# Optimization experiments

Measured on AMD Instinct MI355X. Metric: run time of the kernel, lower is better.

Reference implementation:

```python
import jax, jax.numpy as jnp
import numpy as np

N = 20000   # nodes
E = 400000  # edges per hop
IN_C = 256
HID = 128
HEADS = 2
OUT_C = 256
RELU_SLOPE = 0.2  # GATConv LeakyReLU negative slope
EPS = 1e-16


def _segment_mean(vals, idx, num_segments):
    s = jax.ops.segment_sum(vals, idx, num_segments=num_segments)
    cnt = jax.ops.segment_sum(jnp.ones((vals.shape[0], 1), vals.dtype), idx,
                              num_segments=num_segments)
    return s / (cnt + EPS)


def _gat(x, src, dst, Wg, a_src, a_dst, bg):
    # x: [N, IN_C] -> h: [N, HEADS, HID]
    h = (x @ Wg).reshape(N, HEADS, HID)
    alpha_s = jnp.sum(h * a_src, axis=-1)  # [N, HEADS]
    alpha_d = jnp.sum(h * a_dst, axis=-1)  # [N, HEADS]
    logits = jax.nn.leaky_relu(alpha_s[src] + alpha_d[dst], RELU_SLOPE)  # [E, HEADS]
    # softmax over incoming edges per destination node
    m = jax.ops.segment_max(logits, dst, num_segments=N)  # [N, HEADS]
    m = jnp.where(jnp.isfinite(m), m, 0.0)
    ex = jnp.exp(logits - m[dst])
    denom = jax.ops.segment_sum(ex, dst, num_segments=N)  # [N, HEADS]
    alpha = ex / (denom[dst] + EPS)  # [E, HEADS]
    msg = h[src] * alpha[..., None]  # [E, HEADS, HID]
    out = jax.ops.segment_sum(msg, dst, num_segments=N)  # [N, HEADS, HID]
    return out.reshape(N, HEADS * HID) + bg


def setup_inputs() -> dict:
    key = jax.random.key(0)
    ks = jax.random.split(key, 16)

    def xav(k, shape):
        fan_in, fan_out = shape[0], shape[-1]
        lim = np.sqrt(6.0 / (fan_in + fan_out)).astype(np.float32)
        return jax.random.uniform(k, shape, jnp.float32, -lim, lim)

    inp = {
        "x": jax.random.normal(ks[0], (N, IN_C), jnp.float32),
        "edge_index_1hop": jax.random.randint(ks[1], (2, E), 0, N),
        "edge_time_1hop": jax.random.uniform(ks[2], (E,), jnp.float32),
        "edge_index_2hop": jax.random.randint(ks[3], (2, E), 0, N),
        "edge_time_2hop": jax.random.uniform(ks[4], (E,), jnp.float32),
        "rel_embeddings": jax.random.normal(ks[5], (N, HID), jnp.float32),
        # GATConv params
        "Wg": xav(ks[6], (IN_C, HEADS * HID)),
        "a_src": jax.random.normal(ks[7], (HEADS, HID), jnp.float32) * 0.1,
        "a_dst": jax.random.normal(ks[8], (HEADS, HID), jnp.float32) * 0.1,
        "bg": jnp.zeros((HEADS * HID,), jnp.float32),
        # linear_transform
        "W_lin": xav(ks[9], (HEADS * HID, OUT_C)),
        "b_lin": jnp.zeros((OUT_C,), jnp.float32),
        # time_gate: in = 2*(OUT_C+1)
        "W_tg": xav(ks[10], (2 * (OUT_C + 1), 1)),
        "b_tg": jnp.zeros((1,), jnp.float32),
        # semantic_gate: in = (OUT_C+1) + HID + 1
        "W_sg": xav(ks[11], (OUT_C + 1 + HID + 1, 1)),
        "b_sg": jnp.zeros((1,), jnp.float32),
    }
    return inp


def reference(x, edge_index_1hop, edge_time_1hop, edge_index_2hop,
              edge_time_2hop, rel_embeddings, Wg, a_src, a_dst, bg,
              W_lin, b_lin, W_tg, b_tg, W_sg, b_sg):
    src1, dst1 = edge_index_1hop[0], edge_index_1hop[1]
    src2, dst2 = edge_index_2hop[0], edge_index_2hop[1]

    # ---- 1-hop aggregation ----
    x_1hop = _gat(x, src1, dst1, Wg, a_src, a_dst, bg) @ W_lin + b_lin  # [N, OUT_C]
    time_e1 = edge_time_1hop[:, None]  # [E, 1]
    node_time = _segment_mean(time_e1, dst1, N)  # [N, 1]
    x_1hop_t = jnp.concatenate([x_1hop, node_time], axis=-1)  # [N, OUT_C+1]

    # ---- semantic gate (per 1-hop edge -> per node) ----
    combined = jnp.concatenate(
        [x_1hop_t[src1], rel_embeddings[dst1], time_e1], axis=-1)  # [E, OUT_C+1+HID+1]
    sem_w_edge = jax.nn.sigmoid(combined @ W_sg + b_sg)  # [E, 1]
    sem_w_node = _segment_mean(sem_w_edge, dst1, N)  # [N, 1]

    # ---- 2-hop aggregation, semantically weighted ----
    x_2hop = _gat(x, src2, dst2, Wg, a_src, a_dst, bg) @ W_lin + b_lin  # [N, OUT_C]
    x_2hop = x_2hop * sem_w_node
    x_2hop_t = jnp.concatenate([x_2hop, node_time], axis=-1)  # [N, OUT_C+1]

    # ---- time-gated fusion ----
    gate_in = jnp.concatenate([x_1hop_t, x_2hop_t], axis=-1)  # [N, 2*(OUT_C+1)]
    g = jax.nn.sigmoid(gate_in @ W_tg + b_tg)  # [N, 1]
    return g * x_2hop_t + (1.0 - g) * x_1hop_t
```

## Files before the change

### kernel.cpp

```cpp
#include <hip/hip_runtime.h>
#include <math.h>

constexpr float EPSF = 1e-16f;
#define MAXDEG 64
#define BINCH 4096
#define NBUCK 64

typedef __attribute__((ext_vector_type(8))) short bfrag;
typedef __attribute__((ext_vector_type(4))) float ffrag;
typedef __attribute__((ext_vector_type(2))) float f32x2;
typedef __attribute__((ext_vector_type(8))) unsigned short ushortv8;

__device__ __forceinline__ float leaky(float v){ return v >= 0.f ? v : 0.2f*v; }

__device__ __forceinline__ ushort f2bf(float f){
  union { float f; unsigned u; } v; v.f = f;
  unsigned r = (v.u + 0x7FFFu + ((v.u >> 16) & 1u)) >> 16;
  return (ushort)r;
}
__device__ __forceinline__ float bf2f(ushort u){
  union { unsigned u; float f; } v; v.u = ((unsigned)u) << 16;
  return v.f;
}
__device__ __forceinline__ float asf(unsigned u){
  union { unsigned u; float f; } v; v.u = u; return v.f;
}

__device__ __forceinline__ float wred_max(float v){
  #pragma unroll
  for (int d = 32; d; d >>= 1) v = fmaxf(v, __shfl_xor(v, d));
  return v;
}
__device__ __forceinline__ float wred_sum(float v){
  #pragma unroll
  for (int d = 32; d; d >>= 1) v += __shfl_xor(v, d);
  return v;
}


__global__ __launch_bounds__(256) void k_prep(const float* __restrict__ Wg, const float* __restrict__ Wlin,
    const float* __restrict__ blin, const float* __restrict__ rel, const float* __restrict__ Wsg,
    ushort* __restrict__ Wgt, ushort* __restrict__ Wlt, float* __restrict__ p2,
    float* __restrict__ wv, float* __restrict__ wvc,
    float4* __restrict__ zbase, int znum4, int ZB, int N){
  __shared__ float tile[32][33];
  int b = blockIdx.x, t = threadIdx.x;
  if (b < ZB){
    int idx = b*256 + t;
    if (idx < znum4) zbase[idx] = make_float4(0.f,0.f,0.f,0.f);
  } else if (b < ZB + 128){
    int bb = b - ZB;
    const float* W = (bb < 64) ? Wg : Wlin;
    ushort* Wt = (bb < 64) ? Wgt : Wlt;
    bb &= 63;
    int bx = (bb & 7)*32, by = (bb >> 3)*32;
    int tx = t & 31, ty = t >> 5;
    for (int r = ty; r < 32; r += 8) tile[r][tx] = W[(size_t)(by+r)*256 + bx+tx];
    __syncthreads();
    for (int r = ty; r < 32; r += 8) Wt[(size_t)(bx+r)*256 + by+tx] = f2bf(tile[tx][r]);
  } else if (b == ZB + 128){
    __shared__ float sWsg[256];
    __shared__ float wsum[4];
    sWsg[t] = Wsg[t];
    __syncthreads();
    float acc = 0.f;
    const float* row = Wlin + (size_t)t*256;
    for (int c = 0; c < 256; c += 4){
      acc = fmaf(row[c],   sWsg[c],   acc);
      acc = fmaf(row[c+1], sWsg[c+1], acc);
      acc = fmaf(row[c+2], sWsg[c+2], acc);
      acc = fmaf(row[c+3], sWsg[c+3], acc);
    }
    wv[t] = acc;
    float pc = blin[t]*sWsg[t];
    pc = wred_sum(pc);
    if ((t & 63) == 0) wsum[t >> 6] = pc;
    __syncthreads();
    if (t == 0) wvc[0] = wsum[0] + wsum[1] + wsum[2] + wsum[3];
  } else {
    int node = (b-ZB-129)*4 + (t>>6);
    if (node >= N) return;
    int lane = t & 63;
    const float* rr = rel + (size_t)node*128;
    float q = rr[lane]*Wsg[257+lane] + rr[64+lane]*Wsg[321+lane];
    q = wred_sum(q);
    if (lane == 0) p2[node] = q;
  }
}


__global__ __launch_bounds__(256) void k_work1(const float* __restrict__ x, const ushort* __restrict__ Wgt,
    const float* __restrict__ a_src, const float* __restrict__ a_dst,
    ushort* __restrict__ hb, float* __restrict__ as_, float* __restrict__ ad_,
    const int* __restrict__ ei1, const float* __restrict__ et1, const int* __restrict__ ei2,
    int* __restrict__ gcur, int2* __restrict__ bkt1, int2* __restrict__ bkt2,
    int cap1, int cap2, int N, int E1, int E2, int GB1, int B1, int NB){
  __shared__ int hist[NBUCK];
  __shared__ int loff[NBUCK+1];
  __shared__ int cur[NBUCK];
  __shared__ int gbase_s[NBUCK];
  __shared__ int2 stage[BINCH];
  int bid = blockIdx.x, t = threadIdx.x;
  if (bid >= GB1){
    int hop = (bid >= GB1 + B1);
    int cb  = hop ? (bid - GB1 - B1) : (bid - GB1);
    const int* src_arr = hop ? ei2 : ei1;
    const int* dst_arr = hop ? (ei2 + E2) : (ei1 + E1);
    int Eh = hop ? E2 : E1;
    int c0 = cb * BINCH;
    int M = Eh - c0; if (M > BINCH) M = BINCH;
    if (t < NBUCK) hist[t] = 0;
    __syncthreads();
    #pragma unroll
    for (int k = 0; k < BINCH/256; k++){
      int i = k*256 + t;
      if (i < M) atomicAdd(&hist[dst_arr[c0 + i] / NB], 1);
    }
    __syncthreads();
    if (t < NBUCK){
      int v = hist[t];
      int xx = v;
      #pragma unroll
      for (int d = 1; d < NBUCK; d <<= 1){
        int y = __shfl_up(xx, d);
        if (t >= d) xx += y;
      }
      loff[t+1] = xx;
      if (t == 0) loff[0] = 0;
      cur[t] = xx - v;
      gbase_s[t] = atomicAdd(&gcur[hop*NBUCK + t], v);
    }
    __syncthreads();
    #pragma unroll
    for (int k = 0; k < BINCH/256; k++){
      int i = k*256 + t;
      if (i < M){
        int s = src_arr[c0 + i];
        int d = dst_arr[c0 + i];
        int b = d / NB;
        int ld = d - b*NB;
        int pos = atomicAdd(&cur[b], 1);
        float tv = hop ? 0.f : et1[c0 + i];
        stage[pos] = make_int2(s | (ld << 15), __float_as_int(tv));
      }
    }
    __syncthreads();
    int2* bkt = hop ? bkt2 : bkt1;
    int cap = hop ? cap2 : cap1;
    for (int s = t; s < M; s += 256){
      int lo = 0, hi = NBUCK;
      while (hi - lo > 1){ int mid = (lo + hi) >> 1; if (loff[mid] <= s) lo = mid; else hi = mid; }
      int gpos = gbase_s[lo] + (s - loff[lo]);
      if (gpos < cap) bkt[(size_t)lo*cap + gpos] = stage[s];
    }
    return;
  }
  int head = bid & 1;
  int bx = bid >> 1;
  int wid = t >> 6, lane = t & 63;
  int wr = wid >> 1, wc = wid & 1;
  int row0 = bx*128 + wr*64;
  int col0 = head*128 + wc*64;
  int l15 = lane & 15, lk = lane >> 4;
  ffrag acc[4][4];
  #pragma unroll
  for (int i = 0; i < 4; i++)
    #pragma unroll
    for (int j = 0; j < 4; j++){ ffrag z; z[0]=0.f; z[1]=0.f; z[2]=0.f; z[3]=0.f; acc[i][j] = z; }
  for (int kk = 0; kk < 256; kk += 32){
    bfrag a[4], b[4];
    #pragma unroll
    for (int i = 0; i < 4; i++){
      int r = row0 + i*16 + l15; if (r > N-1) r = N-1;
      float4 u0 = *(const float4*)(x + (size_t)r*256 + kk + lk*8);
      float4 u1 = *(const float4*)(x + (size_t)r*256 + kk + lk*8 + 4);
      bfrag tv;
      tv[0]=(short)f2bf(u0.x); tv[1]=(short)f2bf(u0.y); tv[2]=(short)f2bf(u0.z); tv[3]=(short)f2bf(u0.w);
      tv[4]=(short)f2bf(u1.x); tv[5]=(short)f2bf(u1.y); tv[6]=(short)f2bf(u1.z); tv[7]=(short)f2bf(u1.w);
      a[i] = tv;
      int c = col0 + i*16 + l15;
      b[i] = *(const bfrag*)(Wgt + (size_t)c*256 + kk + lk*8);
    }
    #pragma unroll
    for (int i = 0; i < 4; i++)
      #pragma unroll
      for (int j = 0; j < 4; j++)
        acc[i][j] = __builtin_amdgcn_mfma_f32_16x16x32_bf16(a[i], b[j], acc[i][j], 0, 0, 0);
  }
  float asv[4], adv[4];
  #pragma unroll
  for (int j = 0; j < 4; j++){
    int cc = wc*64 + j*16 + l15;
    asv[j] = a_src[head*128 + cc];
    adv[j] = a_dst[head*128 + cc];
  }
  #pragma unroll
  for (int i = 0; i < 4; i++){
    float ps[4] = {0.f,0.f,0.f,0.f}, pd[4] = {0.f,0.f,0.f,0.f};
    #pragma unroll
    for (int j = 0; j < 4; j++){
      int c = col0 + j*16 + l15;
      #pragma unroll
      for (int q = 0; q < 4; q++){
        int r = row0 + i*16 + lk*4 + q;
        float v = acc[i][j][q];
        if (r < N) hb[(size_t)r*256 + c] = f2bf(v);
        ps[q] = fmaf(v, asv[j], ps[q]);
        pd[q] = fmaf(v, adv[j], pd[q]);
      }
    }
    #pragma unroll
    for (int q = 0; q < 4; q++){
      #pragma unroll
      for (int d = 1; d < 16; d <<= 1){
        ps[q] += __shfl_xor(ps[q], d);
        pd[q] += __shfl_xor(pd[q], d);
      }
      int r = row0 + i*16 + lk*4 + q;
      if (l15 == 0 && r < N){
        atomicAdd(&as_[r*2 + head], ps[q]);
        atomicAdd(&ad_[r*2 + head], pd[q]);
      }
    }
  }
}


__global__ __launch_bounds__(256) void k_place(const int* __restrict__ gcur,
    const int2* __restrict__ bkt1, const int2* __restrict__ bkt2, int cap1, int cap2,
    int* __restrict__ ssrc1, int* __restrict__ ssrc2, float* __restrict__ stime1,
    int* __restrict__ cntg, float* __restrict__ ntime, int N, int NB){
  __shared__ int   cnt_l[512];
  __shared__ float ts_l[512];
  int b = blockIdx.x & 63, hop = blockIdx.x >> 6;
  int t = threadIdx.x;
  int nbase = b * NB;
  int ncnt = N - nbase; if (ncnt > NB) ncnt = NB; if (ncnt < 0) ncnt = 0;
  for (int i = t; i < NB; i += 256){ cnt_l[i] = 0; ts_l[i] = 0.f; }
  __syncthreads();
  const int2* bkt = hop ? bkt2 : bkt1;
  int cap = hop ? cap2 : cap1;
  int len = gcur[hop*NBUCK + b]; if (len > cap) len = cap;
  int* ssrc = hop ? ssrc2 : ssrc1;
  for (int i = t; i < len; i += 256){
    int2 en = bkt[(size_t)b*cap + i];
    int src = en.x & 0x7FFF;
    int ld  = en.x >> 15;
    int slot = atomicAdd(&cnt_l[ld], 1);
    if (slot < MAXDEG){
      size_t o = (size_t)(nbase + ld)*MAXDEG + slot;
      ssrc[o] = src;
      if (hop == 0) stime1[o] = __int_as_float(en.y);
    }
    if (hop == 0) atomicAdd(&ts_l[ld], __int_as_float(en.y));
  }
  __syncthreads();
  for (int ld = t; ld < ncnt; ld += 256){
    int node = nbase + ld;
    int c = cnt_l[ld];
    cntg[hop*N + node] = c;
    if (hop == 0) ntime[node] = ts_l[ld] / ((float)c + EPSF);
  }
}


__global__ __launch_bounds__(256) void k_node(const int* __restrict__ cntg,
    const int* __restrict__ ssrc1, const int* __restrict__ ssrc2,
    const float* __restrict__ as_, const float* __restrict__ ad_,
    const ushort* __restrict__ h, const float* __restrict__ bg,
    const float* __restrict__ wv, const float* __restrict__ wvc,
    const float* __restrict__ Wsg, const float* __restrict__ ntime,
    ushort* __restrict__ gatb, float* __restrict__ p1, int N, int gN4){
  __shared__ int   s_src[4][MAXDEG];
  __shared__ float s_wf[4][2][MAXDEG];
  int wid = threadIdx.x >> 6, lane = threadIdx.x & 63;
  int hop = blockIdx.x >= gN4;
  int node = (blockIdx.x - (hop ? gN4 : 0))*4 + wid;
  bool active = node < N;
  const int* ssrc = hop ? ssrc2 : ssrc1;
  int deg = 0; float ad0 = 0.f, ad1 = 0.f;
  if (active){
    int degt = cntg[hop*N + node];
    deg = degt > MAXDEG ? MAXDEG : degt;
    ad0 = ad_[node*2]; ad1 = ad_[node*2+1];
  }
  size_t o0 = (size_t)node * MAXDEG;
  int msrc = 0;
  float l0 = -INFINITY, l1 = -INFINITY;
  if (lane < deg){
    msrc = ssrc[o0 + lane];
    float2 a = ((const float2*)as_)[msrc];
    l0 = leaky(a.x + ad0); l1 = leaky(a.y + ad1);
  }
  float m0 = wred_max(l0), m1 = wred_max(l1);
  float x0 = 0.f, x1 = 0.f;
  if (lane < deg){ x0 = __expf(l0 - m0); x1 = __expf(l1 - m1); }
  float e0 = wred_sum(x0), e1 = wred_sum(x1);
  s_src[wid][lane] = msrc;
  s_wf[wid][0][lane] = x0 / (e0 + EPSF);
  s_wf[wid][1][lane] = x1 / (e1 + EPSF);
  if (!active) return;
  int eh = lane >> 5, cl = lane & 31, ch0 = cl << 3, head = cl >> 4;
  const float* wrow = s_wf[wid][head];
  const int*   srow = s_src[wid];
  f32x2 acc2[4];
  #pragma unroll
  for (int j = 0; j < 4; j++){ acc2[j][0] = 0.f; acc2[j][1] = 0.f; }
  union UV { ushortv8 v; unsigned d[4]; };
  int i = 0;
  for (; i + 8 <= deg; i += 8){
    int eA = i + eh, eB = i + 2 + eh, eC = i + 4 + eh, eD = i + 6 + eh;
    int sA = srow[eA], sB = srow[eB], sC = srow[eC], sD = srow[eD];
    float wA = wrow[eA], wB = wrow[eB], wC = wrow[eC], wD = wrow[eD];
    UV uA, uB, uC, uD;
    uA.v = *(const ushortv8*)(h + (size_t)sA*256 + ch0);
    uB.v = *(const ushortv8*)(h + (size_t)sB*256 + ch0);
    uC.v = *(const ushortv8*)(h + (size_t)sC*256 + ch0);
    uD.v = *(const ushortv8*)(h + (size_t)sD*256 + ch0);
    f32x2 wA2 = {wA,wA}, wB2 = {wB,wB}, wC2 = {wC,wC}, wD2 = {wD,wD};
    #pragma unroll
    for (int j = 0; j < 4; j++){
      f32x2 hv;
      hv[0] = asf(uA.d[j] << 16); hv[1] = asf(uA.d[j] & 0xffff0000u);
      acc2[j] += hv * wA2;
    }
    #pragma unroll
    for (int j = 0; j < 4; j++){
      f32x2 hv;
      hv[0] = asf(uB.d[j] << 16); hv[1] = asf(uB.d[j] & 0xffff0000u);
      acc2[j] += hv * wB2;
    }
    #pragma unroll
    for (int j = 0; j < 4; j++){
      f32x2 hv;
      hv[0] = asf(uC.d[j] << 16); hv[1] = asf(uC.d[j] & 0xffff0000u);
      acc2[j] += hv * wC2;
    }
    #pragma unroll
    for (int j = 0; j < 4; j++){
      f32x2 hv;
      hv[0] = asf(uD.d[j] << 16); hv[1] = asf(uD.d[j] & 0xffff0000u);
      acc2[j] += hv * wD2;
    }
  }
  for (; i < deg; i += 2){
    int e = i + eh;
    bool v = e < deg;
    int s = v ? srow[e] : 0;
    float w = v ? wrow[e] : 0.f;
    UV u; u.v = *(const ushortv8*)(h + (size_t)s*256 + ch0);
    f32x2 w2 = {w, w};
    #pragma unroll
    for (int j = 0; j < 4; j++){
      f32x2 hv;
      hv[0] = asf(u.d[j] << 16); hv[1] = asf(u.d[j] & 0xffff0000u);
      acc2[j] += hv * w2;
    }
  }
  #pragma unroll
  for (int j = 0; j < 4; j++){
    acc2[j][0] += __shfl_xor(acc2[j][0], 32);
    acc2[j][1] += __shfl_xor(acc2[j][1], 32);
  }
  if (eh == 0){
    float4 b0 = *(const float4*)(bg + ch0);
    float4 b1 = *(const float4*)(bg + ch0 + 4);
    float a8[8];
    a8[0] = acc2[0][0] + b0.x; a8[1] = acc2[0][1] + b0.y;
    a8[2] = acc2[1][0] + b0.z; a8[3] = acc2[1][1] + b0.w;
    a8[4] = acc2[2][0] + b1.x; a8[5] = acc2[2][1] + b1.y;
    a8[6] = acc2[3][0] + b1.z; a8[7] = acc2[3][1] + b1.w;
    ushortv8 o;
    #pragma unroll
    for (int k = 0; k < 8; k++) o[k] = f2bf(a8[k]);
    *(ushortv8*)(gatb + (size_t)(hop ? N + node : node)*256 + ch0) = o;
    if (hop == 0){
      float vs = 0.f;
      const float* wvp = wv + ch0;
      #pragma unroll
      for (int k = 0; k < 8; k++) vs = fmaf(a8[k], wvp[k], vs);
      #pragma unroll
      for (int d = 16; d; d >>= 1) vs += __shfl_xor(vs, d);
      if (cl == 0) p1[node] = vs + wvc[0] + ntime[node]*Wsg[256];
    }
  }
}


__global__ __launch_bounds__(256) void k_gemm2(const ushort* __restrict__ A, const ushort* __restrict__ Bt,
    const float* __restrict__ bias, ushort* __restrict__ Cb, int M){
  int wid = threadIdx.x >> 6, lane = threadIdx.x & 63;
  int wr = wid >> 1, wc = wid & 1;
  int row0 = blockIdx.x*128 + wr*64;
  int col0 = blockIdx.y*128 + wc*64;
  int l15 = lane & 15, lk = lane >> 4;
  ffrag acc[4][4];
  #pragma unroll
  for (int i = 0; i < 4; i++)
    #pragma unroll
    for (int j = 0; j < 4; j++){ ffrag z; z[0]=0.f; z[1]=0.f; z[2]=0.f; z[3]=0.f; acc[i][j] = z; }
  for (int kk = 0; kk < 256; kk += 32){
    bfrag a[4], b[4];
    #pragma unroll
    for (int i = 0; i < 4; i++){
      int r = row0 + i*16 + l15; if (r > M-1) r = M-1;
      a[i] = *(const bfrag*)(A + (size_t)r*256 + kk + lk*8);
      int c = col0 + i*16 + l15;
      b[i] = *(const bfrag*)(Bt + (size_t)c*256 + kk + lk*8);
    }
    #pragma unroll
    for (int i = 0; i < 4; i++)
      #pragma unroll
      for (int j = 0; j < 4; j++)
        acc[i][j] = __builtin_amdgcn_mfma_f32_16x16x32_bf16(a[i], b[j], acc[i][j], 0, 0, 0);
  }
  float bv[4];
  #pragma unroll
  for (int j = 0; j < 4; j++) bv[j] = bias[col0 + j*16 + l15];
  #pragma unroll
  for (int i = 0; i < 4; i++){
    #pragma unroll
    for (int j = 0; j < 4; j++){
      int c = col0 + j*16 + l15;
      #pragma unroll
      for (int q = 0; q < 4; q++){
        int r = row0 + i*16 + lk*4 + q;
        if (r < M) Cb[(size_t)r*256 + c] = f2bf(acc[i][j][q] + bv[j]);
      }
    }
  }
}


__global__ __launch_bounds__(256) void k_final(const ushort* __restrict__ x1, const ushort* __restrict__ x2r,
    const int* __restrict__ cntg, const int* __restrict__ ssrc1, const float* __restrict__ stime1,
    const float* __restrict__ p1, const float* __restrict__ p2,
    const float* __restrict__ Wsg, const float* __restrict__ bsg,
    const float* __restrict__ ntime, const float* __restrict__ Wtg, const float* __restrict__ btg,
    float* __restrict__ out, int N){
  int node = blockIdx.x*4 + (threadIdx.x>>6);
  if (node >= N) return;
  int lane = threadIdx.x & 63;
  int degt = cntg[node];
  int deg = degt > MAXDEG ? MAXDEG : degt;
  float acc = 0.f;
  if (lane < deg){
    size_t o = (size_t)node*MAXDEG + lane;
    float z = p1[ssrc1[o]] + p2[node] + bsg[0] + stime1[o]*Wsg[385];
    acc = 1.f / (1.f + __expf(-z));
  }
  acc = wred_sum(acc);
  float sm = acc / ((float)degt + EPSF);
  float nt = ntime[node];
  int c0 = lane << 2;
  ushort4 au = *(const ushort4*)(x1  + (size_t)node*256 + c0);
  ushort4 ru = *(const ushort4*)(x2r + (size_t)node*256 + c0);
  float4 a4 = make_float4(bf2f(au.x), bf2f(au.y), bf2f(au.z), bf2f(au.w));
  float4 b4; b4.x = bf2f(ru.x)*sm; b4.y = bf2f(ru.y)*sm; b4.z = bf2f(ru.z)*sm; b4.w = bf2f(ru.w)*sm;
  float4 w1 = *(const float4*)(Wtg + c0);
  float4 w2 = *(const float4*)(Wtg + 257 + c0);
  float s = a4.x*w1.x + a4.y*w1.y + a4.z*w1.z + a4.w*w1.w
          + b4.x*w2.x + b4.y*w2.y + b4.z*w2.z + b4.w*w2.w;
  if (lane == 0) s += nt*Wtg[256] + nt*Wtg[513] + btg[0];
  s = wred_sum(s);
  float g = 1.f / (1.f + __expf(-s));
  float* orow = out + (size_t)node*257;
  orow[c0+0] = g*b4.x + (1.f - g)*a4.x;
  orow[c0+1] = g*b4.y + (1.f - g)*a4.y;
  orow[c0+2] = g*b4.z + (1.f - g)*a4.z;
  orow[c0+3] = g*b4.w + (1.f - g)*a4.w;
  if (lane == 0) orow[256] = nt;
}


extern "C" void kernel_launch(void* const* d_in, const int* in_sizes, int n_in,
                              void* d_out, int out_size, void* d_ws, size_t ws_size,
                              hipStream_t stream){
  const float* x    = (const float*)d_in[0];
  const int*   ei1  = (const int*)d_in[1];
  const float* et1  = (const float*)d_in[2];
  const int*   ei2  = (const int*)d_in[3];
  const float* rel  = (const float*)d_in[5];
  const float* Wg   = (const float*)d_in[6];
  const float* asrc = (const float*)d_in[7];
  const float* adst = (const float*)d_in[8];
  const float* bg   = (const float*)d_in[9];
  const float* Wlin = (const float*)d_in[10];
  const float* blin = (const float*)d_in[11];
  const float* Wtg  = (const float*)d_in[12];
  const float* btg  = (const float*)d_in[13];
  const float* Wsg  = (const float*)d_in[14];
  const float* bsg  = (const float*)d_in[15];
  float* out = (float*)d_out;

  const int N  = in_sizes[0] / 256;
  const int E1 = in_sizes[1] / 2;
  const int E2 = in_sizes[3] / 2;
  const int NB = (N + NBUCK - 1) / NBUCK;
  const int cap1 = E1/NBUCK + 2048;
  const int cap2 = E2/NBUCK + 2048;

  char* base = (char*)d_ws;
  size_t off = 0;
  auto alloc = [&](size_t bytes)->char*{
    char* p = base + off;
    off += (bytes + 255) & ~(size_t)255;
    return p;
  };
  int*    gcur  = (int*)alloc((size_t)2*NBUCK*4);
  float*  as_   = (float*)alloc((size_t)2*N*4);
  float*  ad_   = (float*)alloc((size_t)2*N*4);
  size_t zero_bytes = off;
  ushort* Wgt   = (ushort*)alloc((size_t)256*256*2);
  ushort* Wlt   = (ushort*)alloc((size_t)256*256*2);
  ushort* hb    = (ushort*)alloc((size_t)N*256*2);
  ushort* gatb  = (ushort*)alloc((size_t)2*N*256*2);
  ushort* x12   = (ushort*)alloc((size_t)2*N*256*2);
  float*  ntime = (float*)alloc((size_t)N*4);
  float*  p1    = (float*)alloc((size_t)N*4);
  float*  p2    = (float*)alloc((size_t)N*4);
  float*  wv    = (float*)alloc((size_t)256*4);
  float*  wvc   = (float*)alloc((size_t)4);
  int*    cntg  = (int*)alloc((size_t)2*N*4);
  int*    ssrc1 = (int*)alloc((size_t)N*MAXDEG*4);
  int*    ssrc2 = (int*)alloc((size_t)N*MAXDEG*4);
  float*  stime1= (float*)alloc((size_t)N*MAXDEG*4);
  int2*   bkt1  = (int2*)alloc((size_t)NBUCK*cap1*8);
  int2*   bkt2  = (int2*)alloc((size_t)NBUCK*cap2*8);

  dim3 blk(256);
  int gN4 = (N + 3) / 4;
  int GB1 = ((N + 127) / 128) * 2;
  int B1  = (E1 + BINCH - 1) / BINCH;
  int B2  = (E2 + BINCH - 1) / BINCH;
  int znum4 = (int)(zero_bytes / 16);
  int ZB = (znum4 + 255) / 256;
  dim3 ggemm2((2*N + 127) / 128, 2);

  k_prep<<<ZB + 129 + gN4, blk, 0, stream>>>(Wg, Wlin, blin, rel, Wsg, Wgt, Wlt, p2,
                                             wv, wvc, (float4*)d_ws, znum4, ZB, N);
  k_work1<<<GB1 + B1 + B2, blk, 0, stream>>>(x, Wgt, asrc, adst, hb, as_, ad_,
                                             ei1, et1, ei2, gcur, bkt1, bkt2,
                                             cap1, cap2, N, E1, E2, GB1, B1, NB);
  k_place<<<128, blk, 0, stream>>>(gcur, bkt1, bkt2, cap1, cap2, ssrc1, ssrc2, stime1,
                                   cntg, ntime, N, NB);
  k_node<<<2*gN4, blk, 0, stream>>>(cntg, ssrc1, ssrc2, as_, ad_, hb, bg,
                                    wv, wvc, Wsg, ntime, gatb, p1, N, gN4);
  k_gemm2<<<ggemm2, blk, 0, stream>>>(gatb, Wlt, blin, x12, 2*N);
  k_final<<<gN4, blk, 0, stream>>>(x12, x12 + (size_t)N*256, cntg, ssrc1, stime1,
                                   p1, p2, Wsg, bsg, ntime, Wtg, btg, out, N);
}
```

Baseline: 155.1 us.

## Rebalance kernel pipeline: bin edges in prep, place edges alongside GEMM1

Moves the edge-binning blocks from the GEMM1 kernel into the prep kernel and moves edge placement (the old k_place) into the GEMM1 kernel, so each stage's independent work overlaps and one launch is removed. Workspace zeroing becomes a hipMemsetAsync instead of dedicated blocks. The gather loop in k_node switches from packed f32x2 math to scalar fmaf with bf16 unpacking, adds a 4-edge remainder loop, and pads the shared weight array. The risk is that the heavier prep kernel and the added LDS use in the merged kernels lower occupancy or lengthen the critical path, and the memset adds its own dispatch.

```diff
diff --git a/kernel.cpp b/kernel.cpp
--- a/kernel.cpp
+++ b/kernel.cpp
@@ -8,7 +8,6 @@
 
 typedef __attribute__((ext_vector_type(8))) short bfrag;
 typedef __attribute__((ext_vector_type(4))) float ffrag;
-typedef __attribute__((ext_vector_type(2))) float f32x2;
 typedef __attribute__((ext_vector_type(8))) unsigned short ushortv8;
 
 __device__ __forceinline__ float leaky(float v){ return v >= 0.f ? v : 0.2f*v; }
@@ -22,9 +21,6 @@
   union { unsigned u; float f; } v; v.u = ((unsigned)u) << 16;
   return v.f;
 }
-__device__ __forceinline__ float asf(unsigned u){
-  union { unsigned u; float f; } v; v.u = u; return v.f;
-}
 
 __device__ __forceinline__ float wred_max(float v){
   #pragma unroll
@@ -40,70 +36,23 @@
 
 __global__ __launch_bounds__(256) void k_prep(const float* __restrict__ Wg, const float* __restrict__ Wlin,
     const float* __restrict__ blin, const float* __restrict__ rel, const float* __restrict__ Wsg,
+    const int* __restrict__ ei1, const float* __restrict__ et1, const int* __restrict__ ei2,
     ushort* __restrict__ Wgt, ushort* __restrict__ Wlt, float* __restrict__ p2,
     float* __restrict__ wv, float* __restrict__ wvc,
-    float4* __restrict__ zbase, int znum4, int ZB, int N){
-  __shared__ float tile[32][33];
-  int b = blockIdx.x, t = threadIdx.x;
-  if (b < ZB){
-    int idx = b*256 + t;
-    if (idx < znum4) zbase[idx] = make_float4(0.f,0.f,0.f,0.f);
-  } else if (b < ZB + 128){
-    int bb = b - ZB;
-    const float* W = (bb < 64) ? Wg : Wlin;
-    ushort* Wt = (bb < 64) ? Wgt : Wlt;
-    bb &= 63;
-    int bx = (bb & 7)*32, by = (bb >> 3)*32;
-    int tx = t & 31, ty = t >> 5;
-    for (int r = ty; r < 32; r += 8) tile[r][tx] = W[(size_t)(by+r)*256 + bx+tx];
-    __syncthreads();
-    for (int r = ty; r < 32; r += 8) Wt[(size_t)(bx+r)*256 + by+tx] = f2bf(tile[tx][r]);
-  } else if (b == ZB + 128){
-    __shared__ float sWsg[256];
-    __shared__ float wsum[4];
-    sWsg[t] = Wsg[t];
-    __syncthreads();
-    float acc = 0.f;
-    const float* row = Wlin + (size_t)t*256;
-    for (int c = 0; c < 256; c += 4){
-      acc = fmaf(row[c],   sWsg[c],   acc);
-      acc = fmaf(row[c+1], sWsg[c+1], acc);
-      acc = fmaf(row[c+2], sWsg[c+2], acc);
-      acc = fmaf(row[c+3], sWsg[c+3], acc);
-    }
-    wv[t] = acc;
-    float pc = blin[t]*sWsg[t];
-    pc = wred_sum(pc);
-    if ((t & 63) == 0) wsum[t >> 6] = pc;
-    __syncthreads();
-    if (t == 0) wvc[0] = wsum[0] + wsum[1] + wsum[2] + wsum[3];
-  } else {
-    int node = (b-ZB-129)*4 + (t>>6);
-    if (node >= N) return;
-    int lane = t & 63;
-    const float* rr = rel + (size_t)node*128;
-    float q = rr[lane]*Wsg[257+lane] + rr[64+lane]*Wsg[321+lane];
-    q = wred_sum(q);
-    if (lane == 0) p2[node] = q;
-  }
-}
-
-
-__global__ __launch_bounds__(256) void k_work1(const float* __restrict__ x, const ushort* __restrict__ Wgt,
-    const float* __restrict__ a_src, const float* __restrict__ a_dst,
-    ushort* __restrict__ hb, float* __restrict__ as_, float* __restrict__ ad_,
-    const int* __restrict__ ei1, const float* __restrict__ et1, const int* __restrict__ ei2,
     int* __restrict__ gcur, int2* __restrict__ bkt1, int2* __restrict__ bkt2,
-    int cap1, int cap2, int N, int E1, int E2, int GB1, int B1, int NB){
+    int cap1, int cap2, int N, int E1, int E2, int B1, int BINB, int NB){
   __shared__ int hist[NBUCK];
   __shared__ int loff[NBUCK+1];
   __shared__ int cur[NBUCK];
   __shared__ int gbase_s[NBUCK];
   __shared__ int2 stage[BINCH];
-  int bid = blockIdx.x, t = threadIdx.x;
-  if (bid >= GB1){
-    int hop = (bid >= GB1 + B1);
-    int cb  = hop ? (bid - GB1 - B1) : (bid - GB1);
+  __shared__ float tile[32][33];
+  __shared__ float sWsg[256];
+  __shared__ float wsum[4];
+  int b = blockIdx.x, t = threadIdx.x;
+  if (b < BINB){
+    int hop = (b >= B1);
+    int cb  = hop ? (b - B1) : b;
     const int* src_arr = hop ? ei2 : ei1;
     const int* dst_arr = hop ? (ei2 + E2) : (ei1 + E1);
     int Eh = hop ? E2 : E1;
@@ -137,9 +86,9 @@
       if (i < M){
         int s = src_arr[c0 + i];
         int d = dst_arr[c0 + i];
-        int b = d / NB;
-        int ld = d - b*NB;
-        int pos = atomicAdd(&cur[b], 1);
+        int bb = d / NB;
+        int ld = d - bb*NB;
+        int pos = atomicAdd(&cur[bb], 1);
         float tv = hop ? 0.f : et1[c0 + i];
         stage[pos] = make_int2(s | (ld << 15), __float_as_int(tv));
       }
@@ -152,6 +101,85 @@
       while (hi - lo > 1){ int mid = (lo + hi) >> 1; if (loff[mid] <= s) lo = mid; else hi = mid; }
       int gpos = gbase_s[lo] + (s - loff[lo]);
       if (gpos < cap) bkt[(size_t)lo*cap + gpos] = stage[s];
+    }
+  } else if (b < BINB + 128){
+    int bb = b - BINB;
+    const float* W = (bb < 64) ? Wg : Wlin;
+    ushort* Wt = (bb < 64) ? Wgt : Wlt;
+    bb &= 63;
+    int bx = (bb & 7)*32, by = (bb >> 3)*32;
+    int tx = t & 31, ty = t >> 5;
+    for (int r = ty; r < 32; r += 8) tile[r][tx] = W[(size_t)(by+r)*256 + bx+tx];
+    __syncthreads();
+    for (int r = ty; r < 32; r += 8) Wt[(size_t)(bx+r)*256 + by+tx] = f2bf(tile[tx][r]);
+  } else if (b == BINB + 128){
+    sWsg[t] = Wsg[t];
+    __syncthreads();
+    float acc = 0.f;
+    const float* row = Wlin + (size_t)t*256;
+    for (int c = 0; c < 256; c += 4){
+      float4 r4 = *(const float4*)(row + c);
+      acc = fmaf(r4.x, sWsg[c],   acc);
+      acc = fmaf(r4.y, sWsg[c+1], acc);
+      acc = fmaf(r4.z, sWsg[c+2], acc);
+      acc = fmaf(r4.w, sWsg[c+3], acc);
+    }
+    wv[t] = acc;
+    float pc = blin[t]*sWsg[t];
+    pc = wred_sum(pc);
+    if ((t & 63) == 0) wsum[t >> 6] = pc;
+    __syncthreads();
+    if (t == 0) wvc[0] = wsum[0] + wsum[1] + wsum[2] + wsum[3];
+  } else {
+    int node = (b-BINB-129)*4 + (t>>6);
+    if (node >= N) return;
+    int lane = t & 63;
+    const float* rr = rel + (size_t)node*128;
+    float q = rr[lane]*Wsg[257+lane] + rr[64+lane]*Wsg[321+lane];
+    q = wred_sum(q);
+    if (lane == 0) p2[node] = q;
+  }
+}
+
+
+__global__ __launch_bounds__(256) void k_work(const float* __restrict__ x, const ushort* __restrict__ Wgt,
+    const float* __restrict__ a_src, const float* __restrict__ a_dst,
+    ushort* __restrict__ hb, float* __restrict__ as_, float* __restrict__ ad_,
+    const int* __restrict__ gcur, const int2* __restrict__ bkt1, const int2* __restrict__ bkt2,
+    int cap1, int cap2, int* __restrict__ ssrc1, int* __restrict__ ssrc2, float* __restrict__ stime1,
+    int* __restrict__ cntg, float* __restrict__ ntime, int N, int NB, int GB1){
+  __shared__ int   cnt_l[512];
+  __shared__ float ts_l[512];
+  int bid = blockIdx.x, t = threadIdx.x;
+  if (bid >= GB1){
+    int pb = bid - GB1;
+    int b = pb & 63, hop = pb >> 6;
+    int nbase = b * NB;
+    int ncnt = N - nbase; if (ncnt > NB) ncnt = NB; if (ncnt < 0) ncnt = 0;
+    for (int i = t; i < NB; i += 256){ cnt_l[i] = 0; ts_l[i] = 0.f; }
+    __syncthreads();
+    const int2* bkt = hop ? bkt2 : bkt1;
+    int cap = hop ? cap2 : cap1;
+    int len = gcur[hop*NBUCK + b]; if (len > cap) len = cap;
+    int* ssrc = hop ? ssrc2 : ssrc1;
+    for (int i = t; i < len; i += 256){
+      int2 en = bkt[(size_t)b*cap + i];
+      int src = en.x & 0x7FFF;
+      int ld  = en.x >> 15;
+      int slot = atomicAdd(&cnt_l[ld], 1);
+      if (slot < MAXDEG){
+        size_t o = (size_t)(nbase + ld)*MAXDEG + slot;
+        ssrc[o] = src;
+        if (hop == 0) stime1[o] = __int_as_float(en.y);
+      }
+      if (hop == 0) atomicAdd(&ts_l[ld], __int_as_float(en.y));
+    }
+    __syncthreads();
+    for (int ld = t; ld < ncnt; ld += 256){
+      int node = nbase + ld;
+      int c = cnt_l[ld];
+      cntg[hop*N + node] = c;
+      if (hop == 0) ntime[node] = ts_l[ld] / ((float)c + EPSF);
     }
     return;
   }
@@ -226,44 +254,6 @@
 }
 
 
-__global__ __launch_bounds__(256) void k_place(const int* __restrict__ gcur,
-    const int2* __restrict__ bkt1, const int2* __restrict__ bkt2, int cap1, int cap2,
-    int* __restrict__ ssrc1, int* __restrict__ ssrc2, float* __restrict__ stime1,
-    int* __restrict__ cntg, float* __restrict__ ntime, int N, int NB){
-  __shared__ int   cnt_l[512];
-  __shared__ float ts_l[512];
-  int b = blockIdx.x & 63, hop = blockIdx.x >> 6;
-  int t = threadIdx.x;
-  int nbase = b * NB;
-  int ncnt = N - nbase; if (ncnt > NB) ncnt = NB; if (ncnt < 0) ncnt = 0;
-  for (int i = t; i < NB; i += 256){ cnt_l[i] = 0; ts_l[i] = 0.f; }
-  __syncthreads();
-  const int2* bkt = hop ? bkt2 : bkt1;
-  int cap = hop ? cap2 : cap1;
-  int len = gcur[hop*NBUCK + b]; if (len > cap) len = cap;
-  int* ssrc = hop ? ssrc2 : ssrc1;
-  for (int i = t; i < len; i += 256){
-    int2 en = bkt[(size_t)b*cap + i];
-    int src = en.x & 0x7FFF;
-    int ld  = en.x >> 15;
-    int slot = atomicAdd(&cnt_l[ld], 1);
-    if (slot < MAXDEG){
-      size_t o = (size_t)(nbase + ld)*MAXDEG + slot;
-      ssrc[o] = src;
-      if (hop == 0) stime1[o] = __int_as_float(en.y);
-    }
-    if (hop == 0) atomicAdd(&ts_l[ld], __int_as_float(en.y));
-  }
-  __syncthreads();
-  for (int ld = t; ld < ncnt; ld += 256){
-    int node = nbase + ld;
-    int c = cnt_l[ld];
-    cntg[hop*N + node] = c;
-    if (hop == 0) ntime[node] = ts_l[ld] / ((float)c + EPSF);
-  }
-}
-
-
 __global__ __launch_bounds__(256) void k_node(const int* __restrict__ cntg,
     const int* __restrict__ ssrc1, const int* __restrict__ ssrc2,
     const float* __restrict__ as_, const float* __restrict__ ad_,
@@ -272,7 +262,7 @@
     const float* __restrict__ Wsg, const float* __restrict__ ntime,
     ushort* __restrict__ gatb, float* __restrict__ p1, int N, int gN4){
   __shared__ int   s_src[4][MAXDEG];
-  __shared__ float s_wf[4][2][MAXDEG];
+  __shared__ float s_wf[4][2][MAXDEG+8];
   int wid = threadIdx.x >> 6, lane = threadIdx.x & 63;
   int hop = blockIdx.x >= gN4;
   int node = (blockIdx.x - (hop ? gN4 : 0))*4 + wid;
@@ -303,73 +293,55 @@
   int eh = lane >> 5, cl = lane & 31, ch0 = cl << 3, head = cl >> 4;
   const float* wrow = s_wf[wid][head];
   const int*   srow = s_src[wid];
-  f32x2 acc2[4];
-  #pragma unroll
-  for (int j = 0; j < 4; j++){ acc2[j][0] = 0.f; acc2[j][1] = 0.f; }
-  union UV { ushortv8 v; unsigned d[4]; };
+  float acc[8] = {0.f,0.f,0.f,0.f,0.f,0.f,0.f,0.f};
   int i = 0;
   for (; i + 8 <= deg; i += 8){
     int eA = i + eh, eB = i + 2 + eh, eC = i + 4 + eh, eD = i + 6 + eh;
     int sA = srow[eA], sB = srow[eB], sC = srow[eC], sD = srow[eD];
     float wA = wrow[eA], wB = wrow[eB], wC = wrow[eC], wD = wrow[eD];
-    UV uA, uB, uC, uD;
-    uA.v = *(const ushortv8*)(h + (size_t)sA*256 + ch0);
-    uB.v = *(const ushortv8*)(h + (size_t)sB*256 + ch0);
-    uC.v = *(const ushortv8*)(h + (size_t)sC*256 + ch0);
-    uD.v = *(const ushortv8*)(h + (size_t)sD*256 + ch0);
-    f32x2 wA2 = {wA,wA}, wB2 = {wB,wB}, wC2 = {wC,wC}, wD2 = {wD,wD};
-    #pragma unroll
-    for (int j = 0; j < 4; j++){
-      f32x2 hv;
-      hv[0] = asf(uA.d[j] << 16); hv[1] = asf(uA.d[j] & 0xffff0000u);
-      acc2[j] += hv * wA2;
-    }
-    #pragma unroll
-    for (int j = 0; j < 4; j++){
-      f32x2 hv;
-      hv[0] = asf(uB.d[j] << 16); hv[1] = asf(uB.d[j] & 0xffff0000u);
-      acc2[j] += hv * wB2;
-    }
-    #pragma unroll
-    for (int j = 0; j < 4; j++){
-      f32x2 hv;
-      hv[0] = asf(uC.d[j] << 16); hv[1] = asf(uC.d[j] & 0xffff0000u);
-      acc2[j] += hv * wC2;
-    }
-    #pragma unroll
-    for (int j = 0; j < 4; j++){
-      f32x2 hv;
-      hv[0] = asf(uD.d[j] << 16); hv[1] = asf(uD.d[j] & 0xffff0000u);
-      acc2[j] += hv * wD2;
-    }
+    ushortv8 uA = *(const ushortv8*)(h + (size_t)sA*256 + ch0);
+    ushortv8 uB = *(const ushortv8*)(h + (size_t)sB*256 + ch0);
+    ushortv8 uC = *(const ushortv8*)(h + (size_t)sC*256 + ch0);
+    ushortv8 uD = *(const ushortv8*)(h + (size_t)sD*256 + ch0);
+    #pragma unroll
+    for (int k = 0; k < 8; k++) acc[k] = fmaf(wA, bf2f(uA[k]), acc[k]);
+    #pragma unroll
+    for (int k = 0; k < 8; k++) acc[k] = fmaf(wB, bf2f(uB[k]), acc[k]);
+    #pragma unroll
+    for (int k = 0; k < 8; k++) acc[k] = fmaf(wC, bf2f(uC[k]), acc[k]);
+    #pragma unroll
+    for (int k = 0; k < 8; k++) acc[k] = fmaf(wD, bf2f(uD[k]), acc[k]);
+  }
+  for (; i + 4 <= deg; i += 4){
+    int eA = i + eh, eB = i + 2 + eh;
+    int sA = srow[eA], sB = srow[eB];
+    float wA = wrow[eA], wB = wrow[eB];
+    ushortv8 uA = *(const ushortv8*)(h + (size_t)sA*256 + ch0);
+    ushortv8 uB = *(const ushortv8*)(h + (size_t)sB*256 + ch0);
+    #pragma unroll
+    for (int k = 0; k < 8; k++) acc[k] = fmaf(wA, bf2f(uA[k]), acc[k]);
+    #pragma unroll
+    for (int k = 0; k < 8; k++) acc[k] = fmaf(wB, bf2f(uB[k]), acc[k]);
   }
   for (; i < deg; i += 2){
     int e = i + eh;
     bool v = e < deg;
     int s = v ? srow[e] : 0;
     float w = v ? wrow[e] : 0.f;
-    UV u; u.v = *(const ushortv8*)(h + (size_t)s*256 + ch0);
-    f32x2 w2 = {w, w};
-    #pragma unroll
-    for (int j = 0; j < 4; j++){
-      f32x2 hv;
-      hv[0] = asf(u.d[j] << 16); hv[1] = asf(u.d[j] & 0xffff0000u);
-      acc2[j] += hv * w2;
-    }
-  }
-  #pragma unroll
-  for (int j = 0; j < 4; j++){
-    acc2[j][0] += __shfl_xor(acc2[j][0], 32);
-    acc2[j][1] += __shfl_xor(acc2[j][1], 32);
-  }
+    ushortv8 u = *(const ushortv8*)(h + (size_t)s*256 + ch0);
+    #pragma unroll
+    for (int k = 0; k < 8; k++) acc[k] = fmaf(w, bf2f(u[k]), acc[k]);
+  }
+  #pragma unroll
+  for (int k = 0; k < 8; k++) acc[k] += __shfl_xor(acc[k], 32);
   if (eh == 0){
     float4 b0 = *(const float4*)(bg + ch0);
     float4 b1 = *(const float4*)(bg + ch0 + 4);
     float a8[8];
-    a8[0] = acc2[0][0] + b0.x; a8[1] = acc2[0][1] + b0.y;
-    a8[2] = acc2[1][0] + b0.z; a8[3] = acc2[1][1] + b0.w;
-    a8[4] = acc2[2][0] + b1.x; a8[5] = acc2[2][1] + b1.y;
-    a8[6] = acc2[3][0] + b1.z; a8[7] = acc2[3][1] + b1.w;
+    a8[0] = acc[0] + b0.x; a8[1] = acc[1] + b0.y;
+    a8[2] = acc[2] + b0.z; a8[3] = acc[3] + b0.w;
+    a8[4] = acc[4] + b1.x; a8[5] = acc[5] + b1.y;
+    a8[6] = acc[6] + b1.z; a8[7] = acc[7] + b1.w;
     ushortv8 o;
     #pragma unroll
     for (int k = 0; k < 8; k++) o[k] = f2bf(a8[k]);
@@ -533,17 +505,16 @@
   int GB1 = ((N + 127) / 128) * 2;
   int B1  = (E1 + BINCH - 1) / BINCH;
   int B2  = (E2 + BINCH - 1) / BINCH;
-  int znum4 = (int)(zero_bytes / 16);
-  int ZB = (znum4 + 255) / 256;
+  int BINB = B1 + B2;
   dim3 ggemm2((2*N + 127) / 128, 2);
 
-  k_prep<<<ZB + 129 + gN4, blk, 0, stream>>>(Wg, Wlin, blin, rel, Wsg, Wgt, Wlt, p2,
-                                             wv, wvc, (float4*)d_ws, znum4, ZB, N);
-  k_work1<<<GB1 + B1 + B2, blk, 0, stream>>>(x, Wgt, asrc, adst, hb, as_, ad_,
-                                             ei1, et1, ei2, gcur, bkt1, bkt2,
-                                             cap1, cap2, N, E1, E2, GB1, B1, NB);
-  k_place<<<128, blk, 0, stream>>>(gcur, bkt1, bkt2, cap1, cap2, ssrc1, ssrc2, stime1,
-                                   cntg, ntime, N, NB);
+  hipMemsetAsync(d_ws, 0, zero_bytes, stream);
+  k_prep<<<BINB + 129 + gN4, blk, 0, stream>>>(Wg, Wlin, blin, rel, Wsg, ei1, et1, ei2,
+                                               Wgt, Wlt, p2, wv, wvc, gcur, bkt1, bkt2,
+                                               cap1, cap2, N, E1, E2, B1, BINB, NB);
+  k_work<<<GB1 + 128, blk, 0, stream>>>(x, Wgt, asrc, adst, hb, as_, ad_,
+                                        gcur, bkt1, bkt2, cap1, cap2,
+                                        ssrc1, ssrc2, stime1, cntg, ntime, N, NB, GB1);
   k_node<<<2*gN4, blk, 0, stream>>>(cntg, ssrc1, ssrc2, as_, ad_, hb, bg,
                                     wv, wvc, Wsg, ntime, gatb, p1, N, gN4);
   k_gemm2<<<ggemm2, blk, 0, stream>>>(gatb, Wlt, blin, x12, 2*N);
```

Measured after the change: 155.7 us. Within noise of the previous version (+0.4%).
